# Optimization experiments

Hardware: AMD Instinct MI355X
Metric: run time of the kernel (lower is better)

## Reference

```python
import jax, jax.numpy as jnp
import numpy as np

NUM_HEADS = 8
KERNEL_SEARCH = 5  # local attention window
EPS = 1e-5


def _layernorm(x, g, b):
    m = jnp.mean(x, axis=-1, keepdims=True)
    v = jnp.var(x, axis=-1, keepdims=True)
    return (x - m) / jnp.sqrt(v + EPS) * g + b


def _unfold3(x):
    # x: [N, C, H, W] -> [N, C*9, H*W]; matches torch F.unfold(kernel=3, pad=1)
    # ordering: channel-major, kernel position (row-major) minor.
    N, C, H, W = x.shape
    xp = jnp.pad(x, ((0, 0), (0, 0), (1, 1), (1, 1)))
    pats = jnp.stack([xp[:, :, i:i + H, j:j + W] for i in range(3) for j in range(3)], axis=2)
    return pats.reshape(N, C * 9, H * W)


def _sai2token(x, w_mlp):
    # x: [b, c, a, h, w] -> tokens [h*w, b*a, spa_dim]
    b, c, a, h, w = x.shape
    x = x.transpose(0, 2, 1, 3, 4).reshape(b * a, c, h, w)
    tok = _unfold3(x).transpose(2, 0, 1)  # [hw, b*a, c*9]
    return jnp.einsum('lnk,ek->lne', tok, w_mlp)


def _local_mask(h, w, k):
    # additive mask [h*w, h*w]: 0 inside local kxk window, -inf outside
    kl, kr = k // 2, k - k // 2
    ii = jnp.arange(h)
    jj = jnp.arange(w)
    okh = (ii[None, :] >= ii[:, None] - kl) & (ii[None, :] < ii[:, None] + kr)  # [h,h]
    okw = (jj[None, :] >= jj[:, None] - kl) & (jj[None, :] < jj[:, None] + kr)  # [w,w]
    ok = okh[:, None, :, None] & okw[None, :, None, :]  # [h,w,h,w]
    ok = ok.reshape(h * w, h * w)
    return jnp.where(ok, 0.0, -jnp.inf).astype(jnp.float32)


def _attention(qk_in, v_in, in_proj_w, out_proj_w, bias):
    # qk_in/v_in: [L, B, E]; torch nn.MultiheadAttention, no biases, eval mode
    L, B, E = qk_in.shape
    Dh = E // NUM_HEADS
    Wq, Wk, Wv = in_proj_w[:E], in_proj_w[E:2 * E], in_proj_w[2 * E:]
    q = jnp.einsum('lbe,fe->lbf', qk_in, Wq).reshape(L, B, NUM_HEADS, Dh)
    k = jnp.einsum('lbe,fe->lbf', qk_in, Wk).reshape(L, B, NUM_HEADS, Dh)
    v = jnp.einsum('lbe,fe->lbf', v_in, Wv).reshape(L, B, NUM_HEADS, Dh)
    scale = 1.0 / np.sqrt(Dh).astype(np.float32)
    scores = jnp.einsum('lbhd,mbhd->bhlm', q, k) * scale + bias[None, None]
    attn = jax.nn.softmax(scores, axis=-1)
    out = jnp.einsum('bhlm,mbhd->lbhd', attn, v).reshape(L, B, E)
    return jnp.einsum('lbe,fe->lbf', out, out_proj_w)


def reference(buffer, spa_position, w_mlp, ln1_g, ln1_b, in_proj_w, out_proj_w,
              ln2_g, ln2_b, ff_w1, ff_w2, conv_w):
    b, c, a, h, w = buffer.shape
    bias = _local_mask(h, w, KERNEL_SEARCH)
    tok = _sai2token(buffer, w_mlp)          # [hw, b*a, E]
    pe = _sai2token(spa_position, w_mlp)
    x = _layernorm(tok + pe, ln1_g, ln1_b)
    tok = _attention(x, tok, in_proj_w, out_proj_w, bias) + tok
    # feed-forward (dropout is identity in eval)
    ff = _layernorm(tok, ln2_g, ln2_b)
    ff = jax.nn.relu(jnp.einsum('lbe,fe->lbf', ff, ff_w1))
    tok = jnp.einsum('lbf,ef->lbe', ff, ff_w2) + tok
    # Token2SAI: '(h w) (b a) e -> b e a h w' then 1x1x1 conv3d
    buf = tok.reshape(h, w, b, a, -1).transpose(2, 4, 3, 0, 1)  # [b, E, a, h, w]
    return jnp.einsum('oe,beahw->boahw', conv_w, buf)


def setup_inputs() -> dict:
    key = jax.random.key(0)
    ks = jax.random.split(key, 8)
    b, c, a, h, w = 1, 64, 25, 32, 32
    E = 2 * c
    s = 0.02
    return {
        'buffer': jax.random.normal(ks[0], (b, c, a, h, w), jnp.float32),
        'spa_position': jax.random.normal(ks[1], (b, c, a, h, w), jnp.float32),
        'w_mlp': jax.random.normal(ks[2], (E, c * 9), jnp.float32) * s,
        'ln1_g': jnp.ones((E,), jnp.float32),
        'ln1_b': jnp.zeros((E,), jnp.float32),
        'in_proj_w': jax.random.normal(ks[3], (3 * E, E), jnp.float32) * s,
        'out_proj_w': jax.random.normal(ks[4], (E, E), jnp.float32) * s,
        'ln2_g': jnp.ones((E,), jnp.float32),
        'ln2_b': jnp.zeros((E,), jnp.float32),
        'ff_w1': jax.random.normal(ks[5], (2 * E, E), jnp.float32) * s,
        'ff_w2': jax.random.normal(ks[6], (E, 2 * E), jnp.float32) * s,
        'conv_w': jax.random.normal(ks[7], (c, E), jnp.float32) * s,
    }
```

## Files before the change

### kernel.cpp

```cpp
#include <hip/hip_runtime.h>
#include <math.h>

#define Lh 32
#define Lw 32
#define LL 1024
#define BN 25
#define EE 128
#define CC 64
#define NHD 8
#define DH 16
#define FFD 256
#define MROWS 25600

typedef __attribute__((ext_vector_type(8))) short short8;
typedef __attribute__((ext_vector_type(4))) float f32x4;

__device__ inline ushort f2b(float x) {
    union { float f; unsigned u; } v; v.f = x;
    unsigned r = (v.u + 0x7fffu + ((v.u >> 16) & 1u)) >> 16;
    return (ushort)r;
}
__device__ inline float b2f(ushort u) {
    union { unsigned u; float f; } v; v.u = ((unsigned)u) << 16;
    return v.f;
}
__device__ inline void unpack8(uint4 p, float* dst) {
    unsigned vals[4] = { p.x, p.y, p.z, p.w };
#pragma unroll
    for (int i = 0; i < 4; i++) {
        union { unsigned u; float f; } lo, hi;
        lo.u = (vals[i] & 0xffffu) << 16;
        hi.u = vals[i] & 0xffff0000u;
        dst[2 * i] = lo.f; dst[2 * i + 1] = hi.f;
    }
}

#define OFF_W2  0
#define OFF_WQK 73728
#define OFF_WV  106496
#define OFF_WO  122880
#define OFF_W1  139264
#define OFF_W2F 172032
#define OFF_WC  204800
#define W_TOTAL 212992

__global__ __launch_bounds__(256) void k_prep_w(
    const float* __restrict__ w_mlp, const float* __restrict__ in_proj,
    const float* __restrict__ out_proj, const float* __restrict__ ff_w1,
    const float* __restrict__ ff_w2, const float* __restrict__ conv_w,
    ushort* __restrict__ Wb)
{
    int i = blockIdx.x * 256 + threadIdx.x;
    if (i >= W_TOTAL) return;
    if (i < 73728) {
        int e = i / 576, k = i - e * 576;
        int tap = k >> 6, ch = k & 63;
        Wb[OFF_W2 + i] = f2b(w_mlp[e * 576 + ch * 9 + tap]);
        return;
    }
    i -= 73728;
    if (i < 32768) { Wb[OFF_WQK + i] = f2b(in_proj[i]); return; }
    i -= 32768;
    if (i < 16384) { Wb[OFF_WV + i] = f2b(in_proj[32768 + i]); return; }
    i -= 16384;
    if (i < 16384) {
        int e = i >> 7, kpos = i & 127;
        int c = kpos >> 5, q = (kpos >> 3) & 3, ii = kpos & 7;
        int orig = (2 * c + (ii >> 2)) * 16 + q * 4 + (ii & 3);
        Wb[OFF_WO + i] = f2b(out_proj[e * 128 + orig]);
        return;
    }
    i -= 16384;
    if (i < 32768) { Wb[OFF_W1 + i] = f2b(ff_w1[i]); return; }
    i -= 32768;
    if (i < 32768) {
        int e = i >> 8, kpos = i & 255;
        int c = kpos >> 5, q = (kpos >> 3) & 3, ii = kpos & 7;
        int orig = (2 * c + (ii >> 2)) * 16 + q * 4 + (ii & 3);
        Wb[OFF_W2F + i] = f2b(ff_w2[e * 256 + orig]);
        return;
    }
    i -= 32768;
    {
        int o = i >> 7, kpos = i & 127;
        int c = kpos >> 5, q = (kpos >> 3) & 3, ii = kpos & 7;
        int orig = (2 * c + (ii >> 2)) * 16 + q * 4 + (ii & 3);
        Wb[OFF_WC + i] = f2b(conv_w[o * 128 + orig]);
    }
}

__global__ __launch_bounds__(256) void k_prep_in(
    const float* __restrict__ buf, const float* __restrict__ spa,
    ushort* __restrict__ T, ushort* __restrict__ S)
{
    const int n = blockIdx.x, y = blockIdx.y;
    __shared__ float t0[64][33];
    __shared__ float t1[64][33];
    const int t = threadIdx.x;
    {
        int ch = t >> 2, x8 = (t & 3) * 8;
        const float* p = buf + ((size_t)(ch * BN + n) * LL + y * Lw + x8);
        const float* q = spa + ((size_t)(ch * BN + n) * LL + y * Lw + x8);
        float4 a0 = ((const float4*)p)[0], a1 = ((const float4*)p)[1];
        float4 b0 = ((const float4*)q)[0], b1 = ((const float4*)q)[1];
        float* d0 = &t0[ch][x8];
        float* d1 = &t1[ch][x8];
        d0[0] = a0.x; d0[1] = a0.y; d0[2] = a0.z; d0[3] = a0.w;
        d0[4] = a1.x; d0[5] = a1.y; d0[6] = a1.z; d0[7] = a1.w;
        d1[0] = a0.x + b0.x; d1[1] = a0.y + b0.y; d1[2] = a0.z + b0.z; d1[3] = a0.w + b0.w;
        d1[4] = a1.x + b1.x; d1[5] = a1.y + b1.y; d1[6] = a1.z + b1.z; d1[7] = a1.w + b1.w;
    }
    __syncthreads();
    {
        int x = t >> 3, c8 = (t & 7) * 8;
        union { ushort u[8]; uint4 v; } o0, o1;
#pragma unroll
        for (int j = 0; j < 8; j++) { o0.u[j] = f2b(t0[c8 + j][x]); o1.u[j] = f2b(t1[c8 + j][x]); }
        size_t base = (((size_t)n * Lh + y) * Lw + x) * 64 + c8;
        *(uint4*)(T + base) = o0.v;
        *(uint4*)(S + base) = o1.v;
    }
}

__global__ __launch_bounds__(256) void k_tok_qkv(
    const ushort* __restrict__ T, const ushort* __restrict__ S,
    const ushort* __restrict__ W2, const ushort* __restrict__ WQK,
    const ushort* __restrict__ WV, const float* __restrict__ g1,
    const float* __restrict__ b1, ushort* __restrict__ TOKb,
    ushort* __restrict__ Qh, ushort* __restrict__ Kh, ushort* __restrict__ VTg)
{
    const int bid = blockIdx.x;
    const int idx = (bid & 7) * 100 + (bid >> 3);
    const int n = idx / 32, y = idx & 31;
    __shared__ ushort At[3 * 34 * 72];
    __shared__ ushort As_[3 * 34 * 72];
    __shared__ ushort Xs[32 * 136];
    __shared__ ushort Vs[32 * 136];
    __shared__ float2 red[32][4];
    const int t = threadIdx.x;
    const uint4 z = make_uint4(0, 0, 0, 0);

    {
        int x = t >> 3, c8 = (t & 7) * 8;
#pragma unroll
        for (int dy = 0; dy < 3; dy++) {
            int yy = y + dy - 1;
            uint4 va = z, vs = z;
            if (yy >= 0 && yy < Lh) {
                size_t gi = (((size_t)n * Lh + yy) * Lw + x) * 64 + c8;
                va = *(const uint4*)(T + gi);
                vs = *(const uint4*)(S + gi);
            }
            *(uint4*)(At + (dy * 34 + x + 1) * 72 + c8) = va;
            *(uint4*)(As_ + (dy * 34 + x + 1) * 72 + c8) = vs;
        }
        if (t < 48) {
            int dy = t / 16, rem = t % 16;
            int colp = (rem >> 3) * 33, c8p = (rem & 7) * 8;
            *(uint4*)(At + (dy * 34 + colp) * 72 + c8p) = z;
            *(uint4*)(As_ + (dy * 34 + colp) * 72 + c8p) = z;
        }
    }
    __syncthreads();

    const int w = t >> 6, lane = t & 63;
    const int col = lane & 15, quad = lane >> 4;
    f32x4 accT[2][2] = {}, accS[2][2] = {};

    for (int tap = 0; tap < 9; tap++) {
        int dy = tap / 3, dx = tap % 3;
#pragma unroll
        for (int cc = 0; cc < 2; cc++) {
            int kg = tap * 64 + cc * 32 + quad * 8;
            short8 b0 = *(const short8*)(W2 + (size_t)(w * 32 + col) * 576 + kg);
            short8 bq = *(const short8*)(W2 + (size_t)(w * 32 + 16 + col) * 576 + kg);
            int abase = (dy * 34 + col + dx) * 72 + cc * 32 + quad * 8;
            short8 aT0 = *(const short8*)(At + abase);
            short8 aT1 = *(const short8*)(At + abase + 16 * 72);
            short8 aS0 = *(const short8*)(As_ + abase);
            short8 aS1 = *(const short8*)(As_ + abase + 16 * 72);
            accT[0][0] = __builtin_amdgcn_mfma_f32_16x16x32_bf16(aT0, b0, accT[0][0], 0, 0, 0);
            accT[0][1] = __builtin_amdgcn_mfma_f32_16x16x32_bf16(aT0, bq, accT[0][1], 0, 0, 0);
            accT[1][0] = __builtin_amdgcn_mfma_f32_16x16x32_bf16(aT1, b0, accT[1][0], 0, 0, 0);
            accT[1][1] = __builtin_amdgcn_mfma_f32_16x16x32_bf16(aT1, bq, accT[1][1], 0, 0, 0);
            accS[0][0] = __builtin_amdgcn_mfma_f32_16x16x32_bf16(aS0, b0, accS[0][0], 0, 0, 0);
            accS[0][1] = __builtin_amdgcn_mfma_f32_16x16x32_bf16(aS0, bq, accS[0][1], 0, 0, 0);
            accS[1][0] = __builtin_amdgcn_mfma_f32_16x16x32_bf16(aS1, b0, accS[1][0], 0, 0, 0);
            accS[1][1] = __builtin_amdgcn_mfma_f32_16x16x32_bf16(aS1, bq, accS[1][1], 0, 0, 0);
        }
    }

#pragma unroll
    for (int mi = 0; mi < 2; mi++)
#pragma unroll
        for (int r = 0; r < 4; r++) {
            float a0 = accS[mi][0][r], a1 = accS[mi][1][r];
            float ss = a0 + a1, qq = a0 * a0 + a1 * a1;
#pragma unroll
            for (int m = 1; m < 16; m <<= 1) {
                ss += __shfl_xor(ss, m, 64);
                qq += __shfl_xor(qq, m, 64);
            }
            if (col == 0) red[mi * 16 + quad * 4 + r][w] = make_float2(ss, qq);
        }
    __syncthreads();

    const float ga = g1[w * 32 + col],      ba = b1[w * 32 + col];
    const float gb = g1[w * 32 + 16 + col], bb = b1[w * 32 + 16 + col];
#pragma unroll
    for (int mi = 0; mi < 2; mi++)
#pragma unroll
        for (int r = 0; r < 4; r++) {
            int x = mi * 16 + quad * 4 + r;
            float2 p0 = red[x][0], p1 = red[x][1], p2 = red[x][2], p3 = red[x][3];
            float mean = (p0.x + p1.x + p2.x + p3.x) * (1.f / 128.f);
            float var  = (p0.y + p1.y + p2.y + p3.y) * (1.f / 128.f) - mean * mean;
            float rstd = rsqrtf(var + 1e-5f);
            int e0 = w * 32 + col, e1 = w * 32 + 16 + col;
            Xs[x * 136 + e0] = f2b((accS[mi][0][r] - mean) * rstd * ga + ba);
            Xs[x * 136 + e1] = f2b((accS[mi][1][r] - mean) * rstd * gb + bb);
            Vs[x * 136 + e0] = f2b(accT[mi][0][r]);
            Vs[x * 136 + e1] = f2b(accT[mi][1][r]);
        }
    __syncthreads();

    short8 xb[2][4], xv[2][4];
#pragma unroll
    for (int j = 0; j < 2; j++)
#pragma unroll
        for (int kc = 0; kc < 4; kc++) {
            xb[j][kc] = *(const short8*)(Xs + (j * 16 + col) * 136 + kc * 32 + quad * 8);
            xv[j][kc] = *(const short8*)(Vs + (j * 16 + col) * 136 + kc * 32 + quad * 8);
        }
    f32x4 Q[2][2] = {}, K[2][2] = {}, V[2][2] = {};
#pragma unroll
    for (int hj = 0; hj < 2; hj++) {
        int h = 2 * w + hj;
#pragma unroll
        for (int kc = 0; kc < 4; kc++) {
            short8 aq = *(const short8*)(WQK + (size_t)(h * 16 + col) * 128 + kc * 32 + quad * 8);
            short8 ak = *(const short8*)(WQK + (size_t)(128 + h * 16 + col) * 128 + kc * 32 + quad * 8);
            short8 av = *(const short8*)(WV + (size_t)(h * 16 + col) * 128 + kc * 32 + quad * 8);
#pragma unroll
            for (int j = 0; j < 2; j++) {
                Q[hj][j] = __builtin_amdgcn_mfma_f32_16x16x32_bf16(aq, xb[j][kc], Q[hj][j], 0, 0, 0);
                K[hj][j] = __builtin_amdgcn_mfma_f32_16x16x32_bf16(ak, xb[j][kc], K[hj][j], 0, 0, 0);
                V[hj][j] = __builtin_amdgcn_mfma_f32_16x16x32_bf16(av, xv[j][kc], V[hj][j], 0, 0, 0);
            }
        }
    }
#pragma unroll
    for (int hj = 0; hj < 2; hj++) {
        int h = 2 * w + hj;
        size_t vrow = ((size_t)(n * 8 + h) * 32 + y) * 512;
#pragma unroll
        for (int j = 0; j < 2; j++) {
            int l = y * 32 + j * 16 + col;
            size_t base = ((size_t)(n * 8 + h) * 1024 + l) * 16 + quad * 4;
            ushort4 oq, ok;
            oq.x = f2b(Q[hj][j][0]); oq.y = f2b(Q[hj][j][1]); oq.z = f2b(Q[hj][j][2]); oq.w = f2b(Q[hj][j][3]);
            ok.x = f2b(K[hj][j][0]); ok.y = f2b(K[hj][j][1]); ok.z = f2b(K[hj][j][2]); ok.w = f2b(K[hj][j][3]);
            *(ushort4*)(Qh + base) = oq;
            *(ushort4*)(Kh + base) = ok;
            int xp = ((col >> 2) << 3) + (j << 2) + (col & 3);
#pragma unroll
            for (int r = 0; r < 4; r++)
                VTg[vrow + (quad * 4 + r) * 32 + xp] = f2b(V[hj][j][r]);
        }
    }
#pragma unroll
    for (int k = 0; k < 2; k++) {
        int idx2 = t + k * 256;
        int r = idx2 >> 4, seg = idx2 & 15;
        *(uint4*)(TOKb + ((size_t)((y * 32 + r) * 25 + n)) * 128 + seg * 8) =
            *(const uint4*)(Vs + r * 136 + seg * 8);
    }
}

__global__ __launch_bounds__(256) void k_attn_oln(
    const ushort* __restrict__ Qh, const ushort* __restrict__ Kh,
    const ushort* __restrict__ VTg, const ushort* __restrict__ WOP,
    const float* __restrict__ g2, const float* __restrict__ b2,
    ushort* __restrict__ TOKb, ushort* __restrict__ XLN2)
{
    __shared__ ushort OX[16 * 136];
    __shared__ ushort Rs[16 * 136];
    __shared__ float2 red[16][4];
    const int bid = blockIdx.x;
    const int idx = (bid & 7) * 200 + (bid >> 3);
    const int n = idx / 64, rem = idx & 63;
    const int y = rem >> 1, half = rem & 1;
    const int t = threadIdx.x, w = t >> 6, lane = t & 63;
    const int col = lane & 15, quad = lane >> 4;

    {
        int r = t >> 4, seg = t & 15;
        *(uint4*)(Rs + r * 136 + seg * 8) =
            *(const uint4*)(TOKb + ((size_t)((y * 32 + half * 16 + r) * 25 + n)) * 128 + seg * 8);
    }

    short8 z8 = {0, 0, 0, 0, 0, 0, 0, 0};
    const int qx = half * 16 + col;
    f32x4 O2[2] = {};
#pragma unroll
    for (int hj = 0; hj < 2; hj++) {
        const int h = 2 * w + hj;
        const size_t base = (size_t)(n * 8 + h) * 1024;
        const size_t vbase = ((size_t)(n * 8 + h) * 32) * 512;

        short8 qf = z8;
        if (quad < 2)
            qf = *(const short8*)(Qh + (base + y * 32 + half * 16 + col) * 16 + quad * 8);

        f32x4 Sc[10] = {};
#pragma unroll
        for (int tt = 0; tt < 10; tt++) {
            int kr = tt >> 1, kx = ((tt & 1) << 4) + col;
            int yyc = min(max(y - 2 + kr, 0), 31);
            short8 kf = z8;
            if (quad < 2)
                kf = *(const short8*)(Kh + (base + yyc * 32 + kx) * 16 + quad * 8);
            Sc[tt] = __builtin_amdgcn_mfma_f32_16x16x32_bf16(kf, qf, Sc[tt], 0, 0, 0);
        }

        float mx = -1e30f;
#pragma unroll
        for (int tt = 0; tt < 10; tt++) {
            int yy = y - 2 + (tt >> 1);
            bool rok = (yy >= 0) && (yy < 32);
            int kxb = ((tt & 1) << 4) + quad * 4;
#pragma unroll
            for (int r = 0; r < 4; r++) {
                int dd = kxb + r - qx;
                bool ok = rok && ((unsigned)(dd + 2) <= 4u);
                float v = ok ? Sc[tt][r] * 0.25f : -1e30f;
                Sc[tt][r] = v;
                mx = fmaxf(mx, v);
            }
        }
        mx = fmaxf(mx, __shfl_xor(mx, 16, 64));
        mx = fmaxf(mx, __shfl_xor(mx, 32, 64));
        float sum = 0.f;
#pragma unroll
        for (int tt = 0; tt < 10; tt++)
#pragma unroll
            for (int r = 0; r < 4; r++) {
                float p = __expf(Sc[tt][r] - mx);
                Sc[tt][r] = p;
                sum += p;
            }
        sum += __shfl_xor(sum, 16, 64);
        sum += __shfl_xor(sum, 32, 64);
        const float inv = 1.f / sum;

#pragma unroll
        for (int c = 0; c < 5; c++) {
            int yyc = min(max(y - 2 + c, 0), 31);
            short8 vt = *(const short8*)(VTg + vbase + (size_t)yyc * 512 + col * 32 + quad * 8);
            union { ushort u[8]; short8 s; } pb;
#pragma unroll
            for (int i = 0; i < 8; i++)
                pb.u[i] = f2b(Sc[2 * c + (i >> 2)][i & 3] * inv);
            O2[hj] = __builtin_amdgcn_mfma_f32_16x16x32_bf16(vt, pb.s, O2[hj], 0, 0, 0);
        }
    }

    {
        union { ushort u[8]; uint4 v; } pb;
#pragma unroll
        for (int i = 0; i < 8; i++)
            pb.u[i] = f2b(O2[i >> 2][i & 3]);
        *(uint4*)(OX + col * 136 + w * 32 + quad * 8) = pb.v;
    }
    __syncthreads();

    f32x4 Y[2] = {};
#pragma unroll
    for (int kc = 0; kc < 4; kc++) {
        short8 hb = *(const short8*)(OX + col * 136 + kc * 32 + quad * 8);
#pragma unroll
        for (int jj = 0; jj < 2; jj++) {
            int et = 2 * w + jj;
            short8 a = *(const short8*)(WOP + (size_t)(et * 16 + col) * 128 + kc * 32 + quad * 8);
            Y[jj] = __builtin_amdgcn_mfma_f32_16x16x32_bf16(a, hb, Y[jj], 0, 0, 0);
        }
    }
    float sum = 0.f, sq = 0.f;
#pragma unroll
    for (int jj = 0; jj < 2; jj++)
#pragma unroll
        for (int r = 0; r < 4; r++) {
            int e = (2 * w + jj) * 16 + quad * 4 + r;
            float v = Y[jj][r] + b2f(Rs[col * 136 + e]);
            Y[jj][r] = v;
            sum += v; sq += v * v;
        }
    sum += __shfl_xor(sum, 16, 64); sum += __shfl_xor(sum, 32, 64);
    sq  += __shfl_xor(sq, 16, 64);  sq  += __shfl_xor(sq, 32, 64);
    if (quad == 0) red[col][w] = make_float2(sum, sq);
    __syncthreads();

    float2 p0 = red[col][0], p1 = red[col][1], p2 = red[col][2], p3 = red[col][3];
    float mean = (p0.x + p1.x + p2.x + p3.x) * (1.f / 128.f);
    float var  = (p0.y + p1.y + p2.y + p3.y) * (1.f / 128.f) - mean * mean;
    float rstd = rsqrtf(var + 1e-5f);
#pragma unroll
    for (int jj = 0; jj < 2; jj++)
#pragma unroll
        for (int r = 0; r < 4; r++) {
            int e = (2 * w + jj) * 16 + quad * 4 + r;
            float v = Y[jj][r];
            Rs[col * 136 + e] = f2b(v);
            OX[col * 136 + e] = f2b((v - mean) * rstd * g2[e] + b2[e]);
        }
    __syncthreads();

    {
        int r = t >> 4, seg = t & 15;
        size_t go = ((size_t)((y * 32 + half * 16 + r) * 25 + n)) * 128 + seg * 8;
        *(uint4*)(TOKb + go) = *(const uint4*)(Rs + r * 136 + seg * 8);
        *(uint4*)(XLN2 + go) = *(const uint4*)(OX + r * 136 + seg * 8);
    }
}

__global__ __launch_bounds__(256) void k_ffn(
    const ushort* __restrict__ XLN2, const ushort* __restrict__ TOKb,
    const ushort* __restrict__ W1, const ushort* __restrict__ W2P,
    const ushort* __restrict__ WCP, float* __restrict__ out)
{
    __shared__ ushort Xs[16 * 136];
    __shared__ float  Rsp[16 * 132];
    __shared__ ushort Hs[16 * 264];
    __shared__ ushort Ys[16 * 136];
    const int b = blockIdx.x, bn = b % 25, l0 = (b / 25) * 16;
    const int t = threadIdx.x, w = t >> 6, lane = t & 63;
    const int col = lane & 15, quad = lane >> 4;

    {
        int r = t >> 4, seg = t & 15;
        size_t m = (size_t)(l0 + r) * 25 + bn;
        *(uint4*)(Xs + r * 136 + seg * 8) = *(const uint4*)(XLN2 + m * 128 + seg * 8);
        uint4 tb = *(const uint4*)(TOKb + m * 128 + seg * 8);
        float fv[8];
        unpack8(tb, fv);
#pragma unroll
        for (int j = 0; j < 8; j++) {
            int e = seg * 8 + j;
            int c = e >> 5, halfb = (e >> 4) & 1, q = (e >> 2) & 3, r2 = e & 3;
            Rsp[r * 132 + c * 32 + q * 8 + halfb * 4 + r2] = fv[j];
        }
    }
    __syncthreads();

    short8 xb[4];
#pragma unroll
    for (int kc = 0; kc < 4; kc++)
        xb[kc] = *(const short8*)(Xs + col * 136 + kc * 32 + quad * 8);

    f32x4 H[4] = {};
#pragma unroll
    for (int j = 0; j < 4; j++) {
        int ft = 4 * w + j;
#pragma unroll
        for (int kc = 0; kc < 4; kc++) {
            short8 a = *(const short8*)(W1 + (size_t)(ft * 16 + col) * 128 + kc * 32 + quad * 8);
            H[j] = __builtin_amdgcn_mfma_f32_16x16x32_bf16(a, xb[kc], H[j], 0, 0, 0);
        }
    }
#pragma unroll
    for (int cc = 0; cc < 2; cc++) {
        union { ushort u[8]; uint4 v; } pb;
#pragma unroll
        for (int i = 0; i < 8; i++)
            pb.u[i] = f2b(fmaxf(H[2 * cc + (i >> 2)][i & 3], 0.f));
        *(uint4*)(Hs + col * 264 + (2 * w + cc) * 32 + quad * 8) = pb.v;
    }
    __syncthreads();

    f32x4 Y[2] = {};
#pragma unroll
    for (int kc = 0; kc < 8; kc++) {
        short8 hb = *(const short8*)(Hs + col * 264 + kc * 32 + quad * 8);
#pragma unroll
        for (int j = 0; j < 2; j++) {
            int et = 2 * w + j;
            short8 a = *(const short8*)(W2P + (size_t)(et * 16 + col) * 256 + kc * 32 + quad * 8);
            Y[j] = __builtin_amdgcn_mfma_f32_16x16x32_bf16(a, hb, Y[j], 0, 0, 0);
        }
    }
    {
        float4 r0 = *(const float4*)(Rsp + col * 132 + w * 32 + quad * 8);
        float4 r1 = *(const float4*)(Rsp + col * 132 + w * 32 + quad * 8 + 4);
        union { ushort u[8]; uint4 v; } pb;
        pb.u[0] = f2b(Y[0][0] + r0.x); pb.u[1] = f2b(Y[0][1] + r0.y);
        pb.u[2] = f2b(Y[0][2] + r0.z); pb.u[3] = f2b(Y[0][3] + r0.w);
        pb.u[4] = f2b(Y[1][0] + r1.x); pb.u[5] = f2b(Y[1][1] + r1.y);
        pb.u[6] = f2b(Y[1][2] + r1.z); pb.u[7] = f2b(Y[1][3] + r1.w);
        *(uint4*)(Ys + col * 136 + w * 32 + quad * 8) = pb.v;
    }
    __syncthreads();

    f32x4 O = {};
#pragma unroll
    for (int c = 0; c < 4; c++) {
        short8 yb = *(const short8*)(Ys + col * 136 + c * 32 + quad * 8);
        short8 a = *(const short8*)(WCP + (size_t)(w * 16 + col) * 128 + c * 32 + quad * 8);
        O = __builtin_amdgcn_mfma_f32_16x16x32_bf16(a, yb, O, 0, 0, 0);
    }
    const int l = l0 + col;
#pragma unroll
    for (int r2 = 0; r2 < 4; r2++) {
        int o = w * 16 + quad * 4 + r2;
        out[(size_t)(o * 25 + bn) * 1024 + l] = O[r2];
    }
}

extern "C" void kernel_launch(void* const* d_in, const int* in_sizes, int n_in,
                              void* d_out, int out_size, void* d_ws, size_t ws_size,
                              hipStream_t stream)
{
    const float* buffer   = (const float*)d_in[0];
    const float* spa      = (const float*)d_in[1];
    const float* w_mlp    = (const float*)d_in[2];
    const float* ln1_g    = (const float*)d_in[3];
    const float* ln1_b    = (const float*)d_in[4];
    const float* in_proj  = (const float*)d_in[5];
    const float* out_proj = (const float*)d_in[6];
    const float* ln2_g    = (const float*)d_in[7];
    const float* ln2_b    = (const float*)d_in[8];
    const float* ff_w1    = (const float*)d_in[9];
    const float* ff_w2    = (const float*)d_in[10];
    const float* conv_w   = (const float*)d_in[11];
    float* out = (float*)d_out;

    char* ws = (char*)d_ws;
    ushort* TOKb = (ushort*)(ws);
    ushort* XLN2 = (ushort*)(ws + 6553600);
    ushort* Qh   = (ushort*)(ws + 13107200);
    ushort* Kh   = (ushort*)(ws + 19660800);
    ushort* VTg  = (ushort*)(ws + 26214400);
    ushort* Tbf  = (ushort*)(ws + 32768000);
    ushort* Sbf  = (ushort*)(ws + 36044800);
    ushort* Wb   = (ushort*)(ws + 39321600);

    k_prep_w<<<dim3((W_TOTAL + 255) / 256), 256, 0, stream>>>(
        w_mlp, in_proj, out_proj, ff_w1, ff_w2, conv_w, Wb);
    k_prep_in<<<dim3(BN, Lh), 256, 0, stream>>>(buffer, spa, Tbf, Sbf);
    k_tok_qkv<<<dim3(800), 256, 0, stream>>>(Tbf, Sbf, Wb + OFF_W2,
                                             Wb + OFF_WQK, Wb + OFF_WV,
                                             ln1_g, ln1_b, TOKb, Qh, Kh, VTg);
    k_attn_oln<<<dim3(1600), 256, 0, stream>>>(Qh, Kh, VTg, Wb + OFF_WO,
                                               ln2_g, ln2_b, TOKb, XLN2);
    k_ffn<<<dim3(1600), 256, 0, stream>>>(XLN2, TOKb, Wb + OFF_W1, Wb + OFF_W2F,
                                          Wb + OFF_WC, out);
}
```

Before: 183.3 us.

## Fuse attention with FFN, merge prep kernels, stage V transpose through LDS

Merges the weight-prep and input-prep kernels into one launch, and fuses the attention/out-proj/LN2 kernel with the FFN and final conv kernel. The post-attention residual now stays in registers instead of round-tripping through global TOKb/XLN2 buffers. The attention scale of 0.25 is folded into the Q weights at prep time. V-transpose stores are staged in shared memory so global writes become coalesced 16-byte stores. In exchange, the fused kernel uses more shared memory and registers, which may lower occupancy.

```diff
diff --git a/kernel.cpp b/kernel.cpp
--- a/kernel.cpp
+++ b/kernel.cpp
@@ -24,16 +24,6 @@
     union { unsigned u; float f; } v; v.u = ((unsigned)u) << 16;
     return v.f;
 }
-__device__ inline void unpack8(uint4 p, float* dst) {
-    unsigned vals[4] = { p.x, p.y, p.z, p.w };
-#pragma unroll
-    for (int i = 0; i < 4; i++) {
-        union { unsigned u; float f; } lo, hi;
-        lo.u = (vals[i] & 0xffffu) << 16;
-        hi.u = vals[i] & 0xffff0000u;
-        dst[2 * i] = lo.f; dst[2 * i + 1] = hi.f;
-    }
-}
 
 #define OFF_W2  0
 #define OFF_WQK 73728
@@ -43,60 +33,64 @@
 #define OFF_W2F 172032
 #define OFF_WC  204800
 #define W_TOTAL 212992
-
-__global__ __launch_bounds__(256) void k_prep_w(
+#define PREPW_BLOCKS 832
+
+__global__ __launch_bounds__(256) void k_prep(
     const float* __restrict__ w_mlp, const float* __restrict__ in_proj,
     const float* __restrict__ out_proj, const float* __restrict__ ff_w1,
     const float* __restrict__ ff_w2, const float* __restrict__ conv_w,
-    ushort* __restrict__ Wb)
+    const float* __restrict__ buf, const float* __restrict__ spa,
+    ushort* __restrict__ Wb, ushort* __restrict__ T, ushort* __restrict__ S)
 {
-    int i = blockIdx.x * 256 + threadIdx.x;
-    if (i >= W_TOTAL) return;
-    if (i < 73728) {
-        int e = i / 576, k = i - e * 576;
-        int tap = k >> 6, ch = k & 63;
-        Wb[OFF_W2 + i] = f2b(w_mlp[e * 576 + ch * 9 + tap]);
-        return;
-    }
-    i -= 73728;
-    if (i < 32768) { Wb[OFF_WQK + i] = f2b(in_proj[i]); return; }
-    i -= 32768;
-    if (i < 16384) { Wb[OFF_WV + i] = f2b(in_proj[32768 + i]); return; }
-    i -= 16384;
-    if (i < 16384) {
-        int e = i >> 7, kpos = i & 127;
-        int c = kpos >> 5, q = (kpos >> 3) & 3, ii = kpos & 7;
-        int orig = (2 * c + (ii >> 2)) * 16 + q * 4 + (ii & 3);
-        Wb[OFF_WO + i] = f2b(out_proj[e * 128 + orig]);
-        return;
-    }
-    i -= 16384;
-    if (i < 32768) { Wb[OFF_W1 + i] = f2b(ff_w1[i]); return; }
-    i -= 32768;
-    if (i < 32768) {
-        int e = i >> 8, kpos = i & 255;
-        int c = kpos >> 5, q = (kpos >> 3) & 3, ii = kpos & 7;
-        int orig = (2 * c + (ii >> 2)) * 16 + q * 4 + (ii & 3);
-        Wb[OFF_W2F + i] = f2b(ff_w2[e * 256 + orig]);
-        return;
-    }
-    i -= 32768;
-    {
-        int o = i >> 7, kpos = i & 127;
-        int c = kpos >> 5, q = (kpos >> 3) & 3, ii = kpos & 7;
-        int orig = (2 * c + (ii >> 2)) * 16 + q * 4 + (ii & 3);
-        Wb[OFF_WC + i] = f2b(conv_w[o * 128 + orig]);
-    }
-}
-
-__global__ __launch_bounds__(256) void k_prep_in(
-    const float* __restrict__ buf, const float* __restrict__ spa,
-    ushort* __restrict__ T, ushort* __restrict__ S)
-{
-    const int n = blockIdx.x, y = blockIdx.y;
     __shared__ float t0[64][33];
     __shared__ float t1[64][33];
     const int t = threadIdx.x;
+    if (blockIdx.x < PREPW_BLOCKS) {
+        int i = blockIdx.x * 256 + t;
+        if (i >= W_TOTAL) return;
+        if (i < 73728) {
+            int e = i / 576, k = i - e * 576;
+            int tap = k >> 6, ch = k & 63;
+            Wb[OFF_W2 + i] = f2b(w_mlp[e * 576 + ch * 9 + tap]);
+            return;
+        }
+        i -= 73728;
+        if (i < 32768) {
+            float v = in_proj[i];
+            Wb[OFF_WQK + i] = f2b(i < 16384 ? v * 0.25f : v);
+            return;
+        }
+        i -= 32768;
+        if (i < 16384) { Wb[OFF_WV + i] = f2b(in_proj[32768 + i]); return; }
+        i -= 16384;
+        if (i < 16384) {
+            int e = i >> 7, kpos = i & 127;
+            int c = kpos >> 5, q = (kpos >> 3) & 3, ii = kpos & 7;
+            int orig = (2 * c + (ii >> 2)) * 16 + q * 4 + (ii & 3);
+            Wb[OFF_WO + i] = f2b(out_proj[e * 128 + orig]);
+            return;
+        }
+        i -= 16384;
+        if (i < 32768) { Wb[OFF_W1 + i] = f2b(ff_w1[i]); return; }
+        i -= 32768;
+        if (i < 32768) {
+            int e = i >> 8, kpos = i & 255;
+            int c = kpos >> 5, q = (kpos >> 3) & 3, ii = kpos & 7;
+            int orig = (2 * c + (ii >> 2)) * 16 + q * 4 + (ii & 3);
+            Wb[OFF_W2F + i] = f2b(ff_w2[e * 256 + orig]);
+            return;
+        }
+        i -= 32768;
+        {
+            int o = i >> 7, kpos = i & 127;
+            int c = kpos >> 5, q = (kpos >> 3) & 3, ii = kpos & 7;
+            int orig = (2 * c + (ii >> 2)) * 16 + q * 4 + (ii & 3);
+            Wb[OFF_WC + i] = f2b(conv_w[o * 128 + orig]);
+        }
+        return;
+    }
+    const int bid = blockIdx.x - PREPW_BLOCKS;
+    const int n = bid >> 5, y = bid & 31;
     {
         int ch = t >> 2, x8 = (t & 3) * 8;
         const float* p = buf + ((size_t)(ch * BN + n) * LL + y * Lw + x8);
@@ -249,10 +243,10 @@
             }
         }
     }
+    ushort* VTs = At;
 #pragma unroll
     for (int hj = 0; hj < 2; hj++) {
         int h = 2 * w + hj;
-        size_t vrow = ((size_t)(n * 8 + h) * 32 + y) * 512;
 #pragma unroll
         for (int j = 0; j < 2; j++) {
             int l = y * 32 + j * 16 + col;
@@ -265,7 +259,7 @@
             int xp = ((col >> 2) << 3) + (j << 2) + (col & 3);
 #pragma unroll
             for (int r = 0; r < 4; r++)
-                VTg[vrow + (quad * 4 + r) * 32 + xp] = f2b(V[hj][j][r]);
+                VTs[(h * 16 + quad * 4 + r) * 34 + xp] = f2b(V[hj][j][r]);
         }
     }
 #pragma unroll
@@ -275,28 +269,46 @@
         *(uint4*)(TOKb + ((size_t)((y * 32 + r) * 25 + n)) * 128 + seg * 8) =
             *(const uint4*)(Vs + r * 136 + seg * 8);
     }
+    __syncthreads();
+    {
+        int h = t >> 5, rem = t & 31, d = rem >> 1, xh = (rem & 1) * 16;
+        size_t vrow = ((size_t)(n * 8 + h) * 32 + y) * 512;
+        union { ushort u[8]; uint4 v; } o0, o1;
+#pragma unroll
+        for (int j = 0; j < 8; j++) {
+            o0.u[j] = VTs[(h * 16 + d) * 34 + xh + j];
+            o1.u[j] = VTs[(h * 16 + d) * 34 + xh + 8 + j];
+        }
+        *(uint4*)(VTg + vrow + d * 32 + xh)     = o0.v;
+        *(uint4*)(VTg + vrow + d * 32 + xh + 8) = o1.v;
+    }
 }
 
-__global__ __launch_bounds__(256) void k_attn_oln(
+__global__ __launch_bounds__(256) void k_attn_ffn(
     const ushort* __restrict__ Qh, const ushort* __restrict__ Kh,
     const ushort* __restrict__ VTg, const ushort* __restrict__ WOP,
     const float* __restrict__ g2, const float* __restrict__ b2,
-    ushort* __restrict__ TOKb, ushort* __restrict__ XLN2)
+    const ushort* __restrict__ W1, const ushort* __restrict__ W2P,
+    const ushort* __restrict__ WCP, const ushort* __restrict__ TOKb,
+    float* __restrict__ out)
 {
     __shared__ ushort OX[16 * 136];
     __shared__ ushort Rs[16 * 136];
+    __shared__ ushort Hs[16 * 264];
+    __shared__ ushort Ys[16 * 136];
     __shared__ float2 red[16][4];
     const int bid = blockIdx.x;
     const int idx = (bid & 7) * 200 + (bid >> 3);
     const int n = idx / 64, rem = idx & 63;
     const int y = rem >> 1, half = rem & 1;
+    const int l0 = y * 32 + half * 16;
     const int t = threadIdx.x, w = t >> 6, lane = t & 63;
     const int col = lane & 15, quad = lane >> 4;
 
     {
         int r = t >> 4, seg = t & 15;
         *(uint4*)(Rs + r * 136 + seg * 8) =
-            *(const uint4*)(TOKb + ((size_t)((y * 32 + half * 16 + r) * 25 + n)) * 128 + seg * 8);
+            *(const uint4*)(TOKb + ((size_t)((l0 + r) * 25 + n)) * 128 + seg * 8);
     }
 
     short8 z8 = {0, 0, 0, 0, 0, 0, 0, 0};
@@ -333,7 +345,7 @@
             for (int r = 0; r < 4; r++) {
                 int dd = kxb + r - qx;
                 bool ok = rok && ((unsigned)(dd + 2) <= 4u);
-                float v = ok ? Sc[tt][r] * 0.25f : -1e30f;
+                float v = ok ? Sc[tt][r] : -1e30f;
                 Sc[tt][r] = v;
                 mx = fmaxf(mx, v);
             }
@@ -400,63 +412,25 @@
     if (quad == 0) red[col][w] = make_float2(sum, sq);
     __syncthreads();
 
-    float2 p0 = red[col][0], p1 = red[col][1], p2 = red[col][2], p3 = red[col][3];
-    float mean = (p0.x + p1.x + p2.x + p3.x) * (1.f / 128.f);
-    float var  = (p0.y + p1.y + p2.y + p3.y) * (1.f / 128.f) - mean * mean;
-    float rstd = rsqrtf(var + 1e-5f);
-#pragma unroll
-    for (int jj = 0; jj < 2; jj++)
-#pragma unroll
-        for (int r = 0; r < 4; r++) {
-            int e = (2 * w + jj) * 16 + quad * 4 + r;
-            float v = Y[jj][r];
-            Rs[col * 136 + e] = f2b(v);
-            OX[col * 136 + e] = f2b((v - mean) * rstd * g2[e] + b2[e]);
-        }
-    __syncthreads();
-
-    {
-        int r = t >> 4, seg = t & 15;
-        size_t go = ((size_t)((y * 32 + half * 16 + r) * 25 + n)) * 128 + seg * 8;
-        *(uint4*)(TOKb + go) = *(const uint4*)(Rs + r * 136 + seg * 8);
-        *(uint4*)(XLN2 + go) = *(const uint4*)(OX + r * 136 + seg * 8);
-    }
-}
-
-__global__ __launch_bounds__(256) void k_ffn(
-    const ushort* __restrict__ XLN2, const ushort* __restrict__ TOKb,
-    const ushort* __restrict__ W1, const ushort* __restrict__ W2P,
-    const ushort* __restrict__ WCP, float* __restrict__ out)
-{
-    __shared__ ushort Xs[16 * 136];
-    __shared__ float  Rsp[16 * 132];
-    __shared__ ushort Hs[16 * 264];
-    __shared__ ushort Ys[16 * 136];
-    const int b = blockIdx.x, bn = b % 25, l0 = (b / 25) * 16;
-    const int t = threadIdx.x, w = t >> 6, lane = t & 63;
-    const int col = lane & 15, quad = lane >> 4;
-
-    {
-        int r = t >> 4, seg = t & 15;
-        size_t m = (size_t)(l0 + r) * 25 + bn;
-        *(uint4*)(Xs + r * 136 + seg * 8) = *(const uint4*)(XLN2 + m * 128 + seg * 8);
-        uint4 tb = *(const uint4*)(TOKb + m * 128 + seg * 8);
-        float fv[8];
-        unpack8(tb, fv);
-#pragma unroll
-        for (int j = 0; j < 8; j++) {
-            int e = seg * 8 + j;
-            int c = e >> 5, halfb = (e >> 4) & 1, q = (e >> 2) & 3, r2 = e & 3;
-            Rsp[r * 132 + c * 32 + q * 8 + halfb * 4 + r2] = fv[j];
-        }
+    {
+        float2 p0 = red[col][0], p1 = red[col][1], p2 = red[col][2], p3 = red[col][3];
+        float mean = (p0.x + p1.x + p2.x + p3.x) * (1.f / 128.f);
+        float var  = (p0.y + p1.y + p2.y + p3.y) * (1.f / 128.f) - mean * mean;
+        float rstd = rsqrtf(var + 1e-5f);
+#pragma unroll
+        for (int jj = 0; jj < 2; jj++)
+#pragma unroll
+            for (int r = 0; r < 4; r++) {
+                int e = (2 * w + jj) * 16 + quad * 4 + r;
+                OX[col * 136 + e] = f2b((Y[jj][r] - mean) * rstd * g2[e] + b2[e]);
+            }
     }
     __syncthreads();
 
     short8 xb[4];
 #pragma unroll
     for (int kc = 0; kc < 4; kc++)
-        xb[kc] = *(const short8*)(Xs + col * 136 + kc * 32 + quad * 8);
-
+        xb[kc] = *(const short8*)(OX + col * 136 + kc * 32 + quad * 8);
     f32x4 H[4] = {};
 #pragma unroll
     for (int j = 0; j < 4; j++) {
@@ -477,7 +451,7 @@
     }
     __syncthreads();
 
-    f32x4 Y[2] = {};
+    f32x4 Y2[2] = {};
 #pragma unroll
     for (int kc = 0; kc < 8; kc++) {
         short8 hb = *(const short8*)(Hs + col * 264 + kc * 32 + quad * 8);
@@ -485,17 +459,14 @@
         for (int j = 0; j < 2; j++) {
             int et = 2 * w + j;
             short8 a = *(const short8*)(W2P + (size_t)(et * 16 + col) * 256 + kc * 32 + quad * 8);
-            Y[j] = __builtin_amdgcn_mfma_f32_16x16x32_bf16(a, hb, Y[j], 0, 0, 0);
-        }
-    }
-    {
-        float4 r0 = *(const float4*)(Rsp + col * 132 + w * 32 + quad * 8);
-        float4 r1 = *(const float4*)(Rsp + col * 132 + w * 32 + quad * 8 + 4);
+            Y2[j] = __builtin_amdgcn_mfma_f32_16x16x32_bf16(a, hb, Y2[j], 0, 0, 0);
+        }
+    }
+    {
         union { ushort u[8]; uint4 v; } pb;
-        pb.u[0] = f2b(Y[0][0] + r0.x); pb.u[1] = f2b(Y[0][1] + r0.y);
-        pb.u[2] = f2b(Y[0][2] + r0.z); pb.u[3] = f2b(Y[0][3] + r0.w);
-        pb.u[4] = f2b(Y[1][0] + r1.x); pb.u[5] = f2b(Y[1][1] + r1.y);
-        pb.u[6] = f2b(Y[1][2] + r1.z); pb.u[7] = f2b(Y[1][3] + r1.w);
+#pragma unroll
+        for (int i = 0; i < 8; i++)
+            pb.u[i] = f2b(Y2[i >> 2][i & 3] + Y[i >> 2][i & 3]);
         *(uint4*)(Ys + col * 136 + w * 32 + quad * 8) = pb.v;
     }
     __syncthreads();
@@ -511,7 +482,7 @@
 #pragma unroll
     for (int r2 = 0; r2 < 4; r2++) {
         int o = w * 16 + quad * 4 + r2;
-        out[(size_t)(o * 25 + bn) * 1024 + l] = O[r2];
+        out[(size_t)(o * 25 + n) * 1024 + l] = O[r2];
     }
 }
 
@@ -535,22 +506,21 @@
 
     char* ws = (char*)d_ws;
     ushort* TOKb = (ushort*)(ws);
-    ushort* XLN2 = (ushort*)(ws + 6553600);
-    ushort* Qh   = (ushort*)(ws + 13107200);
-    ushort* Kh   = (ushort*)(ws + 19660800);
-    ushort* VTg  = (ushort*)(ws + 26214400);
-    ushort* Tbf  = (ushort*)(ws + 32768000);
-    ushort* Sbf  = (ushort*)(ws + 36044800);
-    ushort* Wb   = (ushort*)(ws + 39321600);
-
-    k_prep_w<<<dim3((W_TOTAL + 255) / 256), 256, 0, stream>>>(
-        w_mlp, in_proj, out_proj, ff_w1, ff_w2, conv_w, Wb);
-    k_prep_in<<<dim3(BN, Lh), 256, 0, stream>>>(buffer, spa, Tbf, Sbf);
+    ushort* Qh   = (ushort*)(ws + 6553600);
+    ushort* Kh   = (ushort*)(ws + 13107200);
+    ushort* VTg  = (ushort*)(ws + 19660800);
+    ushort* Tbf  = (ushort*)(ws + 26214400);
+    ushort* Sbf  = (ushort*)(ws + 29491200);
+    ushort* Wb   = (ushort*)(ws + 32768000);
+
+    k_prep<<<dim3(PREPW_BLOCKS + 800), 256, 0, stream>>>(
+        w_mlp, in_proj, out_proj, ff_w1, ff_w2, conv_w,
+        buffer, spa, Wb, Tbf, Sbf);
     k_tok_qkv<<<dim3(800), 256, 0, stream>>>(Tbf, Sbf, Wb + OFF_W2,
                                              Wb + OFF_WQK, Wb + OFF_WV,
                                              ln1_g, ln1_b, TOKb, Qh, Kh, VTg);
-    k_attn_oln<<<dim3(1600), 256, 0, stream>>>(Qh, Kh, VTg, Wb + OFF_WO,
-                                               ln2_g, ln2_b, TOKb, XLN2);
-    k_ffn<<<dim3(1600), 256, 0, stream>>>(XLN2, TOKb, Wb + OFF_W1, Wb + OFF_W2F,
-                                          Wb + OFF_WC, out);
+    k_attn_ffn<<<dim3(1600), 256, 0, stream>>>(Qh, Kh, VTg, Wb + OFF_WO,
+                                               ln2_g, ln2_b, Wb + OFF_W1,
+                                               Wb + OFF_W2F, Wb + OFF_WC,
+                                               TOKb, out);
 }
```

Result: faster. 176.2 us (-3.9%).
